# Performance work log

Hardware: AMD Instinct MI355X
Metric: run time of the kernel (lower is better)

The kernel has to match this reference:

```python
import jax, jax.numpy as jnp
import numpy as np

D_MODEL = 2048
N_HEADS = 16
HEAD_DIM = D_MODEL // N_HEADS
ROPE_THETA = 10000.0
B, S = 2, 2048
MAX_POS = 8192


def _rope(x, position_ids):
    # x: [b, h, s, hd]; position_ids: [b, s] int
    half = HEAD_DIM // 2
    inv_freq = 1.0 / (ROPE_THETA ** (jnp.arange(0, HEAD_DIM, 2, dtype=jnp.float32) / HEAD_DIM))  # [half]
    ang = position_ids[..., None].astype(jnp.float32) * inv_freq  # [b, s, half]
    cos = jnp.concatenate([jnp.cos(ang), jnp.cos(ang)], axis=-1)[:, None]  # [b, 1, s, hd]
    sin = jnp.concatenate([jnp.sin(ang), jnp.sin(ang)], axis=-1)[:, None]
    x1, x2 = x[..., :half], x[..., half:]
    rot = jnp.concatenate([-x2, x1], axis=-1)  # rotate_half
    return x * cos + rot * sin


def setup_inputs() -> dict:
    key = jax.random.key(0)
    ks = jax.random.split(key, 6)
    wscale = 1.0 / np.sqrt(D_MODEL)
    x_sparse = jax.random.normal(ks[0], (B, S, D_MODEL), dtype=jnp.float32)
    Wq = jax.random.normal(ks[1], (D_MODEL, D_MODEL), dtype=jnp.float32) * wscale
    Wk = jax.random.normal(ks[2], (D_MODEL, D_MODEL), dtype=jnp.float32) * wscale
    Wv = jax.random.normal(ks[3], (D_MODEL, D_MODEL), dtype=jnp.float32) * wscale
    Wo = jax.random.normal(ks[4], (D_MODEL, D_MODEL), dtype=jnp.float32) * wscale
    position_ids = jnp.sort(jax.random.randint(ks[5], (B, S), 0, MAX_POS), axis=-1).astype(jnp.int64)
    return {"x_sparse": x_sparse, "Wq": Wq, "Wk": Wk, "Wv": Wv, "Wo": Wo, "position_ids": position_ids}


def reference(x_sparse, Wq, Wk, Wv, Wo, position_ids):
    b, s, d = x_sparse.shape

    def heads(W):
        return (x_sparse @ W).reshape(b, s, N_HEADS, HEAD_DIM).transpose(0, 2, 1, 3)  # [b,h,s,hd]

    q = _rope(heads(Wq), position_ids)
    k = _rope(heads(Wk), position_ids)
    v = heads(Wv)

    scores = jnp.einsum('bhqd,bhkd->bhqk', q, k) / np.float32(np.sqrt(HEAD_DIM))
    # dynamic position-based causal mask: pos_i >= pos_j, broadcast over heads
    mask = position_ids[:, None, :, None] >= position_ids[:, None, None, :]  # [b,1,s,s]
    scores = jnp.where(mask, scores, jnp.float32(-1e30))
    attn = jax.nn.softmax(scores, axis=-1)
    out = jnp.einsum('bhqk,bhkd->bhqd', attn, v)  # [b,h,s,hd]
    out = out.transpose(0, 2, 1, 3).reshape(b, s, d)
    return out @ Wo
```

## Files before the change

### kernel.cpp

```cpp
#include <hip/hip_runtime.h>
#include <stdint.h>


typedef unsigned short u16;
typedef unsigned int u32;
typedef __attribute__((ext_vector_type(8))) short bf16x8;
typedef __attribute__((ext_vector_type(4))) float f32x4;

#define SEQ 2048
#define DM 2048
#define NH 16
#define HD 128
#define SM_SCALE 0.08838834764831845f

__device__ __forceinline__ u16 f2bf(float f) {
  union { float f; uint32_t u; } v; v.f = f;
  uint32_t u = v.u + 0x7fffu + ((v.u >> 16) & 1u);
  return (u16)(u >> 16);
}
__device__ __forceinline__ float bf2f(u16 h) {
  union { uint32_t u; float f; } v; v.u = ((uint32_t)h) << 16; return v.f;
}
__device__ __forceinline__ u32 pack2(float a, float b) {
  return (u32)f2bf(a) | ((u32)f2bf(b) << 16);
}

__device__ __forceinline__ void gl2lds16(const void* g, void* l) {
  __builtin_amdgcn_global_load_lds(
      (const __attribute__((address_space(1))) uint32_t*)g,
      (__attribute__((address_space(3))) uint32_t*)l, 16, 0, 0);
}

__global__ __launch_bounds__(256) void cvt_x(const float* __restrict__ x, u16* __restrict__ xb) {
  int i = blockIdx.x * 256 + threadIdx.x;
  float4 v = ((const float4*)x)[i];
  uint2 r;
  r.x = pack2(v.x, v.y);
  r.y = pack2(v.z, v.w);
  ((uint2*)xb)[i] = r;
}

__global__ __launch_bounds__(256) void wtrans(const float* __restrict__ w0, const float* __restrict__ w1,
                                              const float* __restrict__ w2, const float* __restrict__ w3,
                                              u16* __restrict__ dst) {
  const float* W = blockIdx.z == 0 ? w0 : blockIdx.z == 1 ? w1 : blockIdx.z == 2 ? w2 : w3;
  u16* D = dst + (size_t)blockIdx.z * DM * DM;
  int k0 = blockIdx.x * 32, n0 = blockIdx.y * 32;
  __shared__ u16 t[32][33];
  int tx = threadIdx.x, ty = threadIdx.y;
#pragma unroll
  for (int i = 0; i < 32; i += 8)
    t[ty + i][tx] = f2bf(W[(size_t)(k0 + ty + i) * DM + n0 + tx]);
  __syncthreads();
#pragma unroll
  for (int i = 0; i < 32; i += 8)
    D[(size_t)(n0 + ty + i) * DM + k0 + tx] = t[tx][ty + i];
}

__device__ __forceinline__ void gemm_core(const u16* __restrict__ A, const u16* __restrict__ Bt,
                                          int m0, int n0, u16* As, u16* Bs, f32x4 acc[4][4]) {
  int tid = threadIdx.x, lane = tid & 63;
  int l15 = lane & 15, quad = lane >> 4;
  int wave = tid >> 6;
  int wm = (wave >> 1) * 64, wn = (wave & 1) * 64;
  for (int k0 = 0; k0 < DM; k0 += 64) {
#pragma unroll
    for (int i = 0; i < 4; ++i) {
      int s = i * 256 + tid;
      int row = s >> 3, c = (s & 7) ^ (row & 7);
      gl2lds16(&A[(size_t)(m0 + row) * DM + k0 + c * 8], &As[(s & ~63) * 8]);
      gl2lds16(&Bt[(size_t)(n0 + row) * DM + k0 + c * 8], &Bs[(s & ~63) * 8]);
    }
    __syncthreads();
#pragma unroll
    for (int kk = 0; kk < 2; ++kk) {
      bf16x8 af[4], bfr[4];
#pragma unroll
      for (int mt = 0; mt < 4; ++mt) {
        int row = wm + mt * 16 + l15;
        int c = (kk * 4 + quad) ^ (row & 7);
        af[mt] = *(const bf16x8*)&As[row * 64 + c * 8];
      }
#pragma unroll
      for (int nt = 0; nt < 4; ++nt) {
        int row = wn + nt * 16 + l15;
        int c = (kk * 4 + quad) ^ (row & 7);
        bfr[nt] = *(const bf16x8*)&Bs[row * 64 + c * 8];
      }
#pragma unroll
      for (int mt = 0; mt < 4; ++mt)
#pragma unroll
        for (int nt = 0; nt < 4; ++nt)
          acc[mt][nt] = __builtin_amdgcn_mfma_f32_16x16x32_bf16(af[mt], bfr[nt], acc[mt][nt], 0, 0, 0);
    }
    __syncthreads();
  }
}

__global__ __launch_bounds__(256) void qkv_gemm(const u16* __restrict__ X, const u16* __restrict__ Wt,
                                                u16* __restrict__ Qo, u16* __restrict__ Ko,
                                                u16* __restrict__ Vto) {
  __shared__ u16 As[128 * 64];
  __shared__ u16 Bs[128 * 64];
  const u16* Bt = Wt + (size_t)blockIdx.z * DM * DM;
  int n0 = blockIdx.x * 128, m0 = blockIdx.y * 128;
  f32x4 acc[4][4] = {};
  gemm_core(X, Bt, m0, n0, As, Bs, acc);
  int lane = threadIdx.x & 63, wave = threadIdx.x >> 6;
  int l15 = lane & 15, quad = lane >> 4;
  int wm = (wave >> 1) * 64, wn = (wave & 1) * 64;
  if (blockIdx.z == 2) {
    int h = n0 >> 7;
#pragma unroll
    for (int mt = 0; mt < 4; ++mt)
#pragma unroll
      for (int nt = 0; nt < 4; ++nt) {
        int tok = m0 + wm + mt * 16 + quad * 4;
        int d = wn + nt * 16 + l15;
        int b = tok >> 11, sx = tok & (SEQ - 1);
        u16* dp = &Vto[((size_t)(b * NH + h) * HD + d) * SEQ + sx];
        *(u32*)&dp[0] = pack2(acc[mt][nt][0], acc[mt][nt][1]);
        *(u32*)&dp[2] = pack2(acc[mt][nt][2], acc[mt][nt][3]);
      }
  } else {
    u16* C = blockIdx.z == 0 ? Qo : Ko;
#pragma unroll
    for (int mt = 0; mt < 4; ++mt)
#pragma unroll
      for (int nt = 0; nt < 4; ++nt)
#pragma unroll
        for (int r = 0; r < 4; ++r)
          C[(size_t)(m0 + wm + mt * 16 + quad * 4 + r) * DM + n0 + wn + nt * 16 + l15]
              = f2bf(acc[mt][nt][r]);
  }
}

__global__ __launch_bounds__(256) void proj_gemm(const u16* __restrict__ A, const u16* __restrict__ Wt,
                                                 float* __restrict__ C) {
  __shared__ u16 As[128 * 64];
  __shared__ u16 Bs[128 * 64];
  int n0 = blockIdx.x * 128, m0 = blockIdx.y * 128;
  f32x4 acc[4][4] = {};
  gemm_core(A, Wt, m0, n0, As, Bs, acc);
  int lane = threadIdx.x & 63, wave = threadIdx.x >> 6;
  int l15 = lane & 15, quad = lane >> 4;
  int wm = (wave >> 1) * 64, wn = (wave & 1) * 64;
#pragma unroll
  for (int mt = 0; mt < 4; ++mt)
#pragma unroll
    for (int nt = 0; nt < 4; ++nt)
#pragma unroll
      for (int r = 0; r < 4; ++r)
        C[(size_t)(m0 + wm + mt * 16 + quad * 4 + r) * DM + n0 + wn + nt * 16 + l15] = acc[mt][nt][r];
}

__global__ __launch_bounds__(256) void rope_k(u16* __restrict__ Q, u16* __restrict__ K,
                                              const int* __restrict__ pos) {
  uint32_t idx = blockIdx.x * 256 + threadIdx.x;
  int i = idx & 63;
  int h = (idx >> 6) & 15;
  int s = (idx >> 10) & 2047;
  int b = idx >> 21;
  u16* P = (blockIdx.y == 0) ? Q : K;
  int p = pos[b * SEQ + s];
  float inv = powf(10000.0f, -(float)i * (1.0f / 64.0f));
  float ang = (float)p * inv;
  float sn, cs;
  sincosf(ang, &sn, &cs);
  size_t base = ((size_t)(b * SEQ + s)) * DM + h * HD;
  float x1 = bf2f(P[base + i]), x2 = bf2f(P[base + 64 + i]);
  P[base + i] = f2bf(x1 * cs - x2 * sn);
  P[base + 64 + i] = f2bf(x2 * cs + x1 * sn);
}

__global__ __launch_bounds__(256, 4) void attn_k(const u16* __restrict__ Q, const u16* __restrict__ K,
                                                 const u16* __restrict__ Vt, const int* __restrict__ pos,
                                                 u16* __restrict__ AO) {
  __shared__ u16 Ks[64 * 128];
  __shared__ u16 Vs[128 * 64];
  __shared__ int pk[64];
  int qt = blockIdx.x, bh = blockIdx.y;
  int b = bh >> 4, h = bh & 15;
  int tid = threadIdx.x, lane = tid & 63, wave = tid >> 6;
  int l15 = lane & 15, quad = lane >> 4;
  const int* posb = pos + b * SEQ;
  int q0w = qt * 64 + wave * 16;

  bf16x8 qf[4];
#pragma unroll
  for (int kk = 0; kk < 4; ++kk)
    qf[kk] = *(const bf16x8*)&Q[(size_t)(b * SEQ + q0w + l15) * DM + h * HD + kk * 32 + quad * 8];
  int pq = posb[q0w + l15];
  int pqmax = posb[qt * 64 + 63];

  float m_i = -1.0e30f, l_i = 0.0f;
  f32x4 oacc[8] = {};

  for (int j0 = 0; j0 < SEQ; j0 += 64) {
    if (posb[j0] > pqmax) break;
#pragma unroll
    for (int i = 0; i < 4; ++i) {
      int s = i * 256 + tid;
      { int row = s >> 4, c = (s & 15) ^ (row & 15);
        gl2lds16(&K[(size_t)(b * SEQ + j0 + row) * DM + h * HD + c * 8], &Ks[(s & ~63) * 8]); }
      { int row = s >> 3, c = (s & 7) ^ (row & 7);
        gl2lds16(&Vt[((size_t)(b * NH + h) * HD + row) * SEQ + j0 + c * 8], &Vs[(s & ~63) * 8]); }
    }
    if (tid < 64) pk[tid] = posb[j0 + tid];
    __syncthreads();

    f32x4 sacc[4] = {};
#pragma unroll
    for (int kk = 0; kk < 4; ++kk) {
      bf16x8 kf[4];
#pragma unroll
      for (int kt = 0; kt < 4; ++kt) {
        int row = kt * 16 + l15;
        int c = (kk * 4 + quad) ^ (row & 15);
        kf[kt] = *(const bf16x8*)&Ks[row * 128 + c * 8];
      }
#pragma unroll
      for (int kt = 0; kt < 4; ++kt)
        sacc[kt] = __builtin_amdgcn_mfma_f32_16x16x32_bf16(kf[kt], qf[kk], sacc[kt], 0, 0, 0);
    }

    int4 pkv[4];
#pragma unroll
    for (int kt = 0; kt < 4; ++kt) pkv[kt] = *(const int4*)&pk[kt * 16 + quad * 4];
    float mx = -3.0e38f;
#pragma unroll
    for (int kt = 0; kt < 4; ++kt) {
      const int* pr = (const int*)&pkv[kt];
#pragma unroll
      for (int r = 0; r < 4; ++r) {
        float s = sacc[kt][r] * SM_SCALE;
        s = (pq >= pr[r]) ? s : -1.0e30f;
        sacc[kt][r] = s;
        mx = fmaxf(mx, s);
      }
    }
    mx = fmaxf(mx, __shfl_xor(mx, 16));
    mx = fmaxf(mx, __shfl_xor(mx, 32));
    float mn = fmaxf(m_i, mx);
    float al = __expf(m_i - mn);
    m_i = mn;
    float rs = 0.0f;
    u32 pb[4][2];
#pragma unroll
    for (int kt = 0; kt < 4; ++kt) {
      float p0 = __expf(sacc[kt][0] - mn), p1 = __expf(sacc[kt][1] - mn);
      float p2 = __expf(sacc[kt][2] - mn), p3 = __expf(sacc[kt][3] - mn);
      rs += (p0 + p1) + (p2 + p3);
      pb[kt][0] = pack2(p0, p1);
      pb[kt][1] = pack2(p2, p3);
    }
    rs += __shfl_xor(rs, 16);
    rs += __shfl_xor(rs, 32);
    l_i = l_i * al + rs;
#pragma unroll
    for (int dt = 0; dt < 8; ++dt) oacc[dt] *= al;

    int base0 = l15 + ((quad & 1) << 5);
    bool hi = (quad >> 1) != 0;
#pragma unroll
    for (int kk = 0; kk < 2; ++kk) {
      u32 w[4];
#pragma unroll
      for (int wd = 0; wd < 4; ++wd) {
        int src = base0 + ((wd >> 1) << 4);
        u32 va = __shfl(pb[kk * 2 + 0][wd & 1], src);
        u32 vb = __shfl(pb[kk * 2 + 1][wd & 1], src);
        w[wd] = hi ? vb : va;
      }
      union { bf16x8 v; u32 u[4]; } pt;
      pt.u[0] = w[0]; pt.u[1] = w[1]; pt.u[2] = w[2]; pt.u[3] = w[3];
#pragma unroll
      for (int dt = 0; dt < 8; ++dt) {
        int row = dt * 16 + l15;
        int c = (kk * 4 + quad) ^ (row & 7);
        bf16x8 vf = *(const bf16x8*)&Vs[row * 64 + c * 8];
        oacc[dt] = __builtin_amdgcn_mfma_f32_16x16x32_bf16(vf, pt.v, oacc[dt], 0, 0, 0);
      }
    }
    __syncthreads();
  }

  float inv = 1.0f / l_i;
  u16* aop = &AO[(size_t)(b * SEQ + q0w + l15) * DM + h * HD];
#pragma unroll
  for (int dt = 0; dt < 8; ++dt) {
    int col = dt * 16 + quad * 4;
    *(u32*)&aop[col]     = pack2(oacc[dt][0] * inv, oacc[dt][1] * inv);
    *(u32*)&aop[col + 2] = pack2(oacc[dt][2] * inv, oacc[dt][3] * inv);
  }
}

extern "C" void kernel_launch(void* const* d_in, const int* in_sizes, int n_in,
                              void* d_out, int out_size, void* d_ws, size_t ws_size,
                              hipStream_t stream) {
  const float* x  = (const float*)d_in[0];
  const float* Wq = (const float*)d_in[1];
  const float* Wk = (const float*)d_in[2];
  const float* Wv = (const float*)d_in[3];
  const float* Wo = (const float*)d_in[4];
  const int*  pos = (const int*)d_in[5];
  float* out = (float*)d_out;

  u16* ws  = (u16*)d_ws;
  u16* xb  = ws;
  u16* wt  = xb  + (size_t)4096 * 2048;
  u16* qb  = wt  + (size_t)4 * 2048 * 2048;
  u16* kb  = qb  + (size_t)4096 * 2048;
  u16* vtb = kb  + (size_t)4096 * 2048;
  u16* aob = vtb + (size_t)4096 * 2048;

  cvt_x<<<8192, 256, 0, stream>>>(x, xb);
  wtrans<<<dim3(64, 64, 4), dim3(32, 8), 0, stream>>>(Wq, Wk, Wv, Wo, wt);
  qkv_gemm<<<dim3(16, 32, 3), 256, 0, stream>>>(xb, wt, qb, kb, vtb);
  rope_k<<<dim3(16384, 2), 256, 0, stream>>>(qb, kb, pos);
  attn_k<<<dim3(32, 32), 256, 0, stream>>>(qb, kb, vtb, pos, aob);
  proj_gemm<<<dim3(16, 32), 256, 0, stream>>>(aob, wt + (size_t)3 * 2048 * 2048, out);
}
```

Baseline: 486.4 us.

## Double-buffer K/V tiles in attention and schedule heavy query tiles first

The attention kernel now uses two LDS buffers for K, V and key positions, prefetching the next tile while the current one is computed. This removes one barrier per iteration. Query tiles are launched in reverse order so the longest causal rows start first, and the trip count is computed upfront. LDS use doubles, which lowers occupancy, and the min-blocks launch hint is dropped. The RoPE frequency is computed with exp2f instead of powf.

```diff
diff --git a/kernel.cpp b/kernel.cpp
--- a/kernel.cpp
+++ b/kernel.cpp
@@ -163,7 +163,7 @@
   int b = idx >> 21;
   u16* P = (blockIdx.y == 0) ? Q : K;
   int p = pos[b * SEQ + s];
-  float inv = powf(10000.0f, -(float)i * (1.0f / 64.0f));
+  float inv = exp2f((float)i * -0.20762051f);
   float ang = (float)p * inv;
   float sn, cs;
   sincosf(ang, &sn, &cs);
@@ -173,18 +173,21 @@
   P[base + 64 + i] = f2bf(x2 * cs + x1 * sn);
 }
 
-__global__ __launch_bounds__(256, 4) void attn_k(const u16* __restrict__ Q, const u16* __restrict__ K,
-                                                 const u16* __restrict__ Vt, const int* __restrict__ pos,
-                                                 u16* __restrict__ AO) {
-  __shared__ u16 Ks[64 * 128];
-  __shared__ u16 Vs[128 * 64];
-  __shared__ int pk[64];
-  int qt = blockIdx.x, bh = blockIdx.y;
+__global__ __launch_bounds__(256) void attn_k(const u16* __restrict__ Q, const u16* __restrict__ K,
+                                              const u16* __restrict__ Vt, const int* __restrict__ pos,
+                                              u16* __restrict__ AO) {
+  __shared__ u16 Ks[2][64 * 128];
+  __shared__ u16 Vs[2][128 * 64];
+  __shared__ int pk[2][64];
+  int qt = (int)gridDim.x - 1 - (int)blockIdx.x;
+  int bh = blockIdx.y;
   int b = bh >> 4, h = bh & 15;
   int tid = threadIdx.x, lane = tid & 63, wave = tid >> 6;
   int l15 = lane & 15, quad = lane >> 4;
   const int* posb = pos + b * SEQ;
   int q0w = qt * 64 + wave * 16;
+  const u16* Kbase = &K[(size_t)(b * SEQ) * DM + h * HD];
+  const u16* Vbase = &Vt[(size_t)(b * NH + h) * HD * SEQ];
 
   bf16x8 qf[4];
 #pragma unroll
@@ -193,21 +196,41 @@
   int pq = posb[q0w + l15];
   int pqmax = posb[qt * 64 + 63];
 
-  float m_i = -1.0e30f, l_i = 0.0f;
-  f32x4 oacc[8] = {};
-
-  for (int j0 = 0; j0 < SEQ; j0 += 64) {
-    if (posb[j0] > pqmax) break;
+  int ntile = 1;
+  while (ntile < 32 && posb[ntile * 64] <= pqmax) ++ntile;
+
+  {
+    int j0 = 0;
 #pragma unroll
     for (int i = 0; i < 4; ++i) {
       int s = i * 256 + tid;
       { int row = s >> 4, c = (s & 15) ^ (row & 15);
-        gl2lds16(&K[(size_t)(b * SEQ + j0 + row) * DM + h * HD + c * 8], &Ks[(s & ~63) * 8]); }
+        gl2lds16(&Kbase[(size_t)(j0 + row) * DM + c * 8], &Ks[0][(s & ~63) * 8]); }
       { int row = s >> 3, c = (s & 7) ^ (row & 7);
-        gl2lds16(&Vt[((size_t)(b * NH + h) * HD + row) * SEQ + j0 + c * 8], &Vs[(s & ~63) * 8]); }
-    }
-    if (tid < 64) pk[tid] = posb[j0 + tid];
+        gl2lds16(&Vbase[(size_t)row * SEQ + j0 + c * 8], &Vs[0][(s & ~63) * 8]); }
+    }
+    if (tid < 64) pk[0][tid] = posb[j0 + tid];
+  }
+
+  float m_i = -1.0e30f, l_i = 0.0f;
+  f32x4 oacc[8] = {};
+
+  for (int j = 0; j < ntile; ++j) {
+    int cur = j & 1;
     __syncthreads();
+
+    if (j + 1 < ntile) {
+      int j0n = (j + 1) * 64, alt = cur ^ 1;
+#pragma unroll
+      for (int i = 0; i < 4; ++i) {
+        int s = i * 256 + tid;
+        { int row = s >> 4, c = (s & 15) ^ (row & 15);
+          gl2lds16(&Kbase[(size_t)(j0n + row) * DM + c * 8], &Ks[alt][(s & ~63) * 8]); }
+        { int row = s >> 3, c = (s & 7) ^ (row & 7);
+          gl2lds16(&Vbase[(size_t)row * SEQ + j0n + c * 8], &Vs[alt][(s & ~63) * 8]); }
+      }
+      if (tid < 64) pk[alt][tid] = posb[j0n + tid];
+    }
 
     f32x4 sacc[4] = {};
 #pragma unroll
@@ -217,7 +240,7 @@
       for (int kt = 0; kt < 4; ++kt) {
         int row = kt * 16 + l15;
         int c = (kk * 4 + quad) ^ (row & 15);
-        kf[kt] = *(const bf16x8*)&Ks[row * 128 + c * 8];
+        kf[kt] = *(const bf16x8*)&Ks[cur][row * 128 + c * 8];
       }
 #pragma unroll
       for (int kt = 0; kt < 4; ++kt)
@@ -226,7 +249,7 @@
 
     int4 pkv[4];
 #pragma unroll
-    for (int kt = 0; kt < 4; ++kt) pkv[kt] = *(const int4*)&pk[kt * 16 + quad * 4];
+    for (int kt = 0; kt < 4; ++kt) pkv[kt] = *(const int4*)&pk[cur][kt * 16 + quad * 4];
     float mx = -3.0e38f;
 #pragma unroll
     for (int kt = 0; kt < 4; ++kt) {
@@ -278,11 +301,10 @@
       for (int dt = 0; dt < 8; ++dt) {
         int row = dt * 16 + l15;
         int c = (kk * 4 + quad) ^ (row & 7);
-        bf16x8 vf = *(const bf16x8*)&Vs[row * 64 + c * 8];
+        bf16x8 vf = *(const bf16x8*)&Vs[cur][row * 64 + c * 8];
         oacc[dt] = __builtin_amdgcn_mfma_f32_16x16x32_bf16(vf, pt.v, oacc[dt], 0, 0, 0);
       }
     }
-    __syncthreads();
   }
 
   float inv = 1.0f / l_i;
```

New measurement: 475.9 us. 1.02x faster.
